# Kernel tuning notes

Hardware: AMD Instinct MI355X
Metric: run time of the kernel (lower is better)

The kernel has to match this reference:

```python
import jax, jax.numpy as jnp
import numpy as np

D_MODEL = 2048
N_HEADS = 32
D_HEAD = 64
CHUNK = 128
SEQ = 2048
BZ = 4
LN_EPS = 1e-5
LAYER_IDX = 12
NUM_LAYERS = 24


def _layernorm(x, scale, bias):
    mu = jnp.mean(x, axis=-1, keepdims=True)
    var = jnp.var(x, axis=-1, keepdims=True)
    return (x - mu) * jax.lax.rsqrt(var + LN_EPS) * scale + bias


def setup_inputs() -> dict:
    key = jax.random.key(0)
    ks = jax.random.split(key, 5)
    a01 = LAYER_IDX / (NUM_LAYERS - 1 + 1e-08)
    a10 = 1.0 - LAYER_IDX / NUM_LAYERS
    decay = -8 + 7 * (np.arange(N_HEADS, dtype=np.float64) / (N_HEADS - 1.0 + 1e-07)) ** (0.7 + 1.3 * a01)
    first = np.full((N_HEADS,), -3.0)
    idx = (np.arange(D_MODEL, dtype=np.float64) / D_MODEL).reshape(1, 1, D_MODEL)
    s = 1.0 / np.sqrt(D_MODEL)
    return {
        'inputs': jax.random.normal(ks[0], (BZ, SEQ, D_MODEL), jnp.float32),
        'time_mix_r': jnp.asarray(idx ** (0.5 * a10), jnp.float32),
        'time_mix_k': jnp.asarray(idx ** a10, jnp.float32),
        'time_mix_v': jnp.asarray(idx ** a10 + 0.3 * a01, jnp.float32),
        'key_weight': jax.random.normal(ks[1], (D_MODEL, D_MODEL), jnp.float32) * s,
        'value_weight': jax.random.normal(ks[2], (D_MODEL, D_MODEL), jnp.float32) * s,
        'receptance_weight': jax.random.normal(ks[3], (D_MODEL, D_MODEL), jnp.float32) * s,
        'output_weight': jax.random.normal(ks[4], (D_MODEL, D_MODEL), jnp.float32) * s,
        'time_decay': jnp.asarray(decay, jnp.float32),
        'time_first': jnp.asarray(first, jnp.float32),
        'ln1_scale': jnp.ones((1, 1, D_MODEL), jnp.float32),
        'ln1_bias': jnp.zeros((1, 1, D_MODEL), jnp.float32),
        'lnx_scale': jnp.ones((N_HEADS, D_HEAD), jnp.float32),
        'lnx_bias': jnp.zeros((N_HEADS, D_HEAD), jnp.float32),
        'chunk_size': CHUNK,
    }


def reference(inputs, time_mix_r, time_mix_k, time_mix_v, key_weight, value_weight,
              receptance_weight, output_weight, time_decay, time_first,
              ln1_scale, ln1_bias, lnx_scale, lnx_bias, chunk_size):
    bz, seq, d = inputs.shape
    H = time_decay.shape[0]
    dh = d // H
    C = chunk_size
    nc = seq // C

    xn = _layernorm(inputs, ln1_scale, ln1_bias)

    # decay machinery (matches the TF w_mask / w_k / w_b construction)
    w = jnp.exp(-jnp.exp(time_decay))                       # (H,)
    rev = jnp.arange(C - 1, -1, -1, dtype=jnp.float32)
    w_pow = w[:, None] ** rev[None, :]                      # (H,C): w^(C-1-j)
    w_k = w_pow[:, None, :]                                 # (H,1,C)
    w_b = w_pow[:, ::-1][:, :, None]                        # (H,C,1): w^i
    w_chunk = (w ** C)[:, None, None]                       # (H,1,1)
    u = jnp.exp(time_first)                                 # (H,)
    ii = jnp.arange(C)
    dmat = ii[:, None] - ii[None, :]                        # i - j
    e = jnp.maximum(dmat - 1, 0)
    w_mask = jnp.where(dmat[None] > 0, w[:, None, None] ** e[None],
                       jnp.where(dmat[None] == 0, u[:, None, None], 0.0))  # (H,C,C)
    w_mask = w_mask[None, None]                             # (1,1,H,C,C)

    # token shift mixing (initial state_x = zeros)
    shift = jnp.concatenate([jnp.zeros((bz, 1, d), xn.dtype), xn[:, :-1]], axis=1)
    rx = xn * time_mix_r + (1.0 - time_mix_r) * shift
    kx = xn * time_mix_k + (1.0 - time_mix_k) * shift
    vx = xn * time_mix_v + (1.0 - time_mix_v) * shift

    r = (rx @ receptance_weight).reshape(bz, nc, C, H, dh).transpose(0, 1, 3, 2, 4)  # (bz,nc,H,C,dh)
    k = (kx @ key_weight).reshape(bz, nc, C, H, dh).transpose(0, 1, 3, 4, 2)         # (bz,nc,H,dh,C)
    v = (vx @ value_weight).reshape(bz, nc, C, H, dh).transpose(0, 1, 3, 2, 4)       # (bz,nc,H,C,dh)

    # intra-chunk attention with decay mask
    rkw = (r @ k) * w_mask                                  # (bz,nc,H,C,C)
    sep = rkw @ v                                           # (bz,nc,H,C,dh)

    # inter-chunk recurrent state via scan
    state0 = jnp.zeros((bz, H, dh, dh), inputs.dtype)

    def step(state, rkv):
        rc, kc, vc = rkv                                    # (bz,H,C,dh),(bz,H,dh,C),(bz,H,C,dh)
        bias = (rc @ state) * w_b                           # (bz,H,C,dh)
        new_state = state * w_chunk + (kc * w_k) @ vc
        return new_state, bias

    r_s = jnp.moveaxis(r, 1, 0)
    k_s = jnp.moveaxis(k, 1, 0)
    v_s = jnp.moveaxis(v, 1, 0)
    state, bias = jax.lax.scan(step, state0, (r_s, k_s, v_s))
    bias = jnp.moveaxis(bias, 0, 1)                         # (bz,nc,H,C,dh)

    att = (sep + bias).transpose(0, 1, 3, 2, 4)             # (bz,nc,C,H,dh)
    att = _layernorm(att, lnx_scale, lnx_bias)              # group norm over dh per head
    out = att.reshape(bz, seq, d) @ output_weight
    return inputs + out, xn[:, -1, :], state
```

## Files before the change

### kernel.cpp

```cpp
#include <hip/hip_runtime.h>

#define D_MODEL 2048
#define N_HEADS 32
#define D_HEAD  64
#define CHUNK   128
#define SEQ     2048
#define BZ      4
#define NC      16
#define NTOK    (BZ*SEQ)
#define LN_EPS  1e-5f

typedef __bf16 bf16_t;
typedef bf16_t bf16x8 __attribute__((ext_vector_type(8)));
typedef float  f32x4  __attribute__((ext_vector_type(4)));

#define GLOBAL_AS __attribute__((address_space(1)))
#define LDS_AS    __attribute__((address_space(3)))

__global__ __launch_bounds__(256) void k_ln_mix(
    const float* __restrict__ x, const float* __restrict__ tmr,
    const float* __restrict__ tmk, const float* __restrict__ tmv,
    const float* __restrict__ g1, const float* __restrict__ b1,
    bf16_t* __restrict__ rxb, bf16_t* __restrict__ kxb, bf16_t* __restrict__ vxb,
    float* __restrict__ xn_last)
{
    __shared__ float sbuf[16];
    const int row = blockIdx.x;
    const int t = row & (SEQ-1);
    const int tid = threadIdx.x;
    const float4* xc4 = (const float4*)(x + (size_t)row*D_MODEL);
    float4 c0 = xc4[tid*2], c1 = xc4[tid*2+1];
    float4 p0 = {0,0,0,0}, p1 = {0,0,0,0};
    const bool hasprev = (t != 0);
    if (hasprev){
        const float4* xp4 = (const float4*)(x + (size_t)(row-1)*D_MODEL);
        p0 = xp4[tid*2]; p1 = xp4[tid*2+1];
    }
    float xc[8] = {c0.x,c0.y,c0.z,c0.w,c1.x,c1.y,c1.z,c1.w};
    float xp[8] = {p0.x,p0.y,p0.z,p0.w,p1.x,p1.y,p1.z,p1.w};
    float sc=0.f, qc=0.f, sp=0.f, qp=0.f;
    for (int q=0;q<8;++q){ sc+=xc[q]; qc+=xc[q]*xc[q]; sp+=xp[q]; qp+=xp[q]*xp[q]; }
    for (int o=1;o<64;o<<=1){
        sc += __shfl_xor(sc,o,64); qc += __shfl_xor(qc,o,64);
        sp += __shfl_xor(sp,o,64); qp += __shfl_xor(qp,o,64);
    }
    const int wave = tid>>6, lane = tid&63;
    if (lane==0){ sbuf[wave*4+0]=sc; sbuf[wave*4+1]=qc; sbuf[wave*4+2]=sp; sbuf[wave*4+3]=qp; }
    __syncthreads();
    sc = sbuf[0]+sbuf[4]+sbuf[8]+sbuf[12];
    qc = sbuf[1]+sbuf[5]+sbuf[9]+sbuf[13];
    sp = sbuf[2]+sbuf[6]+sbuf[10]+sbuf[14];
    qp = sbuf[3]+sbuf[7]+sbuf[11]+sbuf[15];
    const float inv = 1.f/(float)D_MODEL;
    float muc = sc*inv, varc = qc*inv - muc*muc;
    float rc  = rsqrtf(varc + LN_EPS);
    float mup = sp*inv, varp = qp*inv - mup*mup;
    float rp  = rsqrtf(varp + LN_EPS);
    bf16x8 rv, kv, vv;
    const int ci = tid*8;
    float xnl[8];
    for (int q=0;q<8;++q){
        int c = ci+q;
        float gg = g1[c], bb = b1[c];
        float xn = (xc[q]-muc)*rc*gg + bb;
        float sh = hasprev ? ((xp[q]-mup)*rp*gg + bb) : 0.f;
        float mr = tmr[c], mk = tmk[c], mv = tmv[c];
        rv[q] = (bf16_t)(xn*mr + (1.f-mr)*sh);
        kv[q] = (bf16_t)(xn*mk + (1.f-mk)*sh);
        vv[q] = (bf16_t)(xn*mv + (1.f-mv)*sh);
        xnl[q] = xn;
    }
    size_t base = (size_t)row*D_MODEL + ci;
    *(bf16x8*)&rxb[base] = rv;
    *(bf16x8*)&kxb[base] = kv;
    *(bf16x8*)&vxb[base] = vv;
    if (t == SEQ-1){
        int b = row >> 11;
        for (int q=0;q<8;++q) xn_last[(size_t)b*D_MODEL + ci + q] = xnl[q];
    }
}

__global__ __launch_bounds__(256) void k_wt4(
    const float* __restrict__ W0, const float* __restrict__ W1,
    const float* __restrict__ W2, const float* __restrict__ W3,
    bf16_t* __restrict__ WTbase)
{
    __shared__ float tile[64][65];
    const int z = blockIdx.z;
    const float* W = (z==0)?W0:(z==1)?W1:(z==2)?W2:W3;
    bf16_t* WT = WTbase + (size_t)z*D_MODEL*D_MODEL;
    const int n0 = blockIdx.x*64, k0 = blockIdx.y*64;
    const int j = threadIdx.x & 63, i0 = threadIdx.x >> 6;
    for (int it=0; it<16; ++it){
        int i = i0 + it*4;
        tile[j][i] = W[(size_t)(k0+i)*D_MODEL + n0 + j];
    }
    __syncthreads();
    for (int it=0; it<16; ++it){
        int idx = threadIdx.x + it*256;
        int r = idx >> 6, c = idx & 63;
        WT[(size_t)(n0+r)*D_MODEL + k0 + c] = (bf16_t)tile[r][c];
    }
}

__device__ __forceinline__ void xcd_swizzle_8x32(int& bx, int& by)
{
    int id = blockIdx.y*8 + blockIdx.x;
    int p  = id & 7;
    int n  = id >> 3;
    bx = n & 7;
    by = (p<<2) | (n>>3);
}

__device__ __forceinline__ bf16x8 ldfrag(const char* regn, int ks, int row, int quad)
{
    return *(const bf16x8*)(regn + ks*16384 + row*64 + (((quad ^ (row>>1)) & 3) << 4));
}

#define GLD(gp, lp) __builtin_amdgcn_global_load_lds((const GLOBAL_AS void*)(gp), (LDS_AS void*)(lp), 16, 0, 0)
#define STAGE2(gp, lb) do{ GLD((gp), (lb)+tid16); GLD((gp)+rowskip, (lb)+8192+tid16); }while(0)
#define BARX() do{ asm volatile("" ::: "memory"); __builtin_amdgcn_s_barrier(); asm volatile("" ::: "memory"); }while(0)
#define WAITV(n) asm volatile("s_waitcnt vmcnt(" #n ")" ::: "memory")
#define MM(CH) do{ \
    _Pragma("unroll") for (int mf=0;mf<4;++mf){ \
    _Pragma("unroll") for (int nf=0;nf<4;++nf)  \
        acc[mf][(CH)*4+nf] = __builtin_amdgcn_mfma_f32_16x16x32_bf16( \
            a[mf], b[nf], acc[mf][(CH)*4+nf], 0,0,0); } }while(0)

template<int OUT_BF16>
__device__ __forceinline__ void gemm256_core(
    const bf16_t* __restrict__ A, const bf16_t* __restrict__ B,
    void* __restrict__ Cout, const float* __restrict__ resid,
    const int N, const int K, char* smem, int bx, int by)
{
    const int tid = threadIdx.x;
    const int lane = tid&63, quad = lane>>4, l15 = lane&15;
    const int wave = tid>>6;
    const int wm = wave>>1, wn = wave&1;
    const int wrow = wm*64, wcol = wn*128;
    const int arow0 = by*256, bcol0 = bx*256;
    const int NT = K>>6;
    const int K2 = K*2;
    const int tid16 = tid*16;

    const int rr  = tid>>2;
    const int kcb = (((tid&3) ^ ((tid>>3)&3)) << 4);
    const char* Ag = (const char*)A + (size_t)(arow0 + rr)*K2 + kcb;
    const char* Bg = (const char*)B + (size_t)(bcol0 + rr)*K2 + kcb;
    const int rowskip = 128*K2;

    char* A0 = smem;             char* B0 = smem + 32768;
    char* A1 = smem + 65536;     char* B1 = smem + 98304;

    STAGE2(Ag,       A0);
    STAGE2(Bg,       B0);
    STAGE2(Ag + 64,  A0 + 16384);
    STAGE2(Bg + 64,  B0 + 16384);
    STAGE2(Ag + 128, A1);
    WAITV(6);
    BARX();

    f32x4 acc[4][8];
    #pragma unroll
    for (int i=0;i<4;++i)
        #pragma unroll
        for (int j=0;j<8;++j) acc[i][j] = (f32x4){0.f,0.f,0.f,0.f};

    bf16x8 a[4], b[4];

    #pragma unroll 2
    for (int t=0; t<NT; ++t){
        const char* As = (t&1) ? A1 : A0;
        const char* Bs = (t&1) ? B1 : B0;
        char* An = (t&1) ? A0 : A1;
        char* Bn = (t&1) ? B0 : B1;
        char* Ac = (t&1) ? A1 : A0;
        const int tn  = (t+1 < NT) ? t+1 : NT-1;
        const int tn2 = (t+2 < NT) ? t+2 : NT-1;
        const char* gA1 = Ag + tn*128;
        const char* gB1 = Bg + tn*128;
        const char* gA2 = Ag + tn2*128;

        #pragma unroll
        for (int mf=0;mf<4;++mf) a[mf] = ldfrag(As, 0, wrow+mf*16+l15, quad);
        #pragma unroll
        for (int nf=0;nf<4;++nf) b[nf] = ldfrag(Bs, 0, wcol+nf*16+l15, quad);
        STAGE2(gB1, Bn);
        BARX();
        __builtin_amdgcn_s_setprio(1); MM(0); __builtin_amdgcn_s_setprio(0);
        BARX();
        #pragma unroll
        for (int nf=0;nf<4;++nf) b[nf] = ldfrag(Bs, 0, wcol+64+nf*16+l15, quad);
        STAGE2(gA1 + 64, An + 16384);
        WAITV(6);
        BARX();
        __builtin_amdgcn_s_setprio(1); MM(1); __builtin_amdgcn_s_setprio(0);
        BARX();
        #pragma unroll
        for (int mf=0;mf<4;++mf) a[mf] = ldfrag(As, 1, wrow+mf*16+l15, quad);
        #pragma unroll
        for (int nf=0;nf<4;++nf) b[nf] = ldfrag(Bs, 1, wcol+nf*16+l15, quad);
        STAGE2(gB1 + 64, Bn + 16384);
        BARX();
        __builtin_amdgcn_s_setprio(1); MM(0); __builtin_amdgcn_s_setprio(0);
        BARX();
        #pragma unroll
        for (int nf=0;nf<4;++nf) b[nf] = ldfrag(Bs, 1, wcol+64+nf*16+l15, quad);
        STAGE2(gA2, Ac);
        WAITV(6);
        BARX();
        __builtin_amdgcn_s_setprio(1); MM(1); __builtin_amdgcn_s_setprio(0);
        BARX();
    }
    WAITV(0);
    __syncthreads();

    if (OUT_BF16){
        bf16_t* Cb = (bf16_t*)Cout;
        bf16_t* Rp = (bf16_t*)smem;
        #pragma unroll
        for (int jh=0; jh<2; ++jh){
            if (wn == jh){
                #pragma unroll
                for (int mf=0;mf<4;++mf)
                    #pragma unroll
                    for (int nf=0;nf<8;++nf)
                        #pragma unroll
                        for (int e=0;e<4;++e){
                            int rrow = wrow + mf*16 + quad*4 + e;
                            Rp[rrow*136 + nf*16 + l15] = (bf16_t)acc[mf][nf][e];
                        }
            }
            __syncthreads();
            for (int it=0; it<8; ++it){
                int idx = tid + it*512;
                int row = idx >> 4, c8 = (idx & 15)*8;
                *(bf16x8*)&Cb[(size_t)(arow0+row)*N + bcol0 + jh*128 + c8] =
                    *(const bf16x8*)&Rp[row*136 + c8];
            }
            __syncthreads();
        }
    } else {
        float* C = (float*)Cout;
        #pragma unroll
        for (int mf=0;mf<4;++mf)
            #pragma unroll
            for (int nf=0;nf<8;++nf)
                #pragma unroll
                for (int e=0;e<4;++e){
                    size_t r = (size_t)(arow0 + wrow + mf*16 + quad*4 + e);
                    size_t c = (size_t)(bcol0 + wcol + nf*16 + l15);
                    C[r*N + c] = resid[r*N + c] + acc[mf][nf][e];
                }
    }
}

__global__ __launch_bounds__(512, 2) void k_gemm_rkv(
    const bf16_t* __restrict__ Abase, const bf16_t* __restrict__ Bbase,
    bf16_t* __restrict__ Cbase)
{
    __shared__ __align__(16) char smem[131072];
    const int z = blockIdx.z;
    const bf16_t* A = Abase + (size_t)z*NTOK*D_MODEL;
    const bf16_t* B = Bbase + (size_t)z*D_MODEL*D_MODEL;
    bf16_t*       C = Cbase + (size_t)z*NTOK*D_MODEL;
    int bx, by; xcd_swizzle_8x32(bx, by);
    gemm256_core<1>(A, B, (void*)C, nullptr, D_MODEL, D_MODEL, smem, bx, by);
}

__global__ __launch_bounds__(512, 2) void k_gemm_out(
    const bf16_t* __restrict__ A, const bf16_t* __restrict__ B,
    float* __restrict__ C, const float* __restrict__ resid)
{
    __shared__ __align__(16) char smem[131072];
    int bx, by; xcd_swizzle_8x32(bx, by);
    gemm256_core<0>(A, B, (void*)C, resid, D_MODEL, D_MODEL, smem, bx, by);
}

__global__ __launch_bounds__(256) void k_chunk_U(
    const bf16_t* __restrict__ kb, const bf16_t* __restrict__ vb,
    const float* __restrict__ td, float* __restrict__ U)
{
    __shared__ __align__(16) bf16_t kT[64*136];
    __shared__ __align__(16) bf16_t vT[64*136];
    const int bid = blockIdx.x;
    const int h = bid & 31, n = (bid>>5)&15, b = bid>>9;
    const int tid = threadIdx.x;
    const int wave = tid>>6, lane = tid&63, quad = lane>>4, l15 = lane&15;
    const size_t row0 = (size_t)b*SEQ + n*CHUNK;
    const int col0 = h*D_HEAD;
    const float lnw = -__expf(td[h]);
    for (int it=0; it<4; ++it){
        int idx = tid + it*256;
        int row = idx>>3, c8 = (idx&7)*8;
        float wj = __expf(lnw * (float)(CHUNK-1-row));
        bf16x8 kv = *(const bf16x8*)&kb[(row0+row)*D_MODEL + col0 + c8];
        bf16x8 vv = *(const bf16x8*)&vb[(row0+row)*D_MODEL + col0 + c8];
        for (int q=0;q<8;++q){
            kT[(c8+q)*136 + row] = (bf16_t)((float)kv[q] * wj);
            vT[(c8+q)*136 + row] = vv[q];
        }
    }
    __syncthreads();
    f32x4 accU[4];
    for (int j=0;j<4;++j) accU[j] = (f32x4){0.f,0.f,0.f,0.f};
    for (int kk=0; kk<4; ++kk){
        bf16x8 af = *(const bf16x8*)&kT[(wave*16+l15)*136 + kk*32 + quad*8];
        bf16x8 bfr[4];
        for (int j=0;j<4;++j) bfr[j] = *(const bf16x8*)&vT[(j*16+l15)*136 + kk*32 + quad*8];
        for (int j=0;j<4;++j)
            accU[j] = __builtin_amdgcn_mfma_f32_16x16x32_bf16(af, bfr[j], accU[j], 0,0,0);
    }
    float* Ub = U + (size_t)bid*(D_HEAD*D_HEAD);
    for (int j=0;j<4;++j) for (int e=0;e<4;++e){
        int ei = wave*16 + quad*4 + e;
        int d  = j*16 + l15;
        Ub[ei*D_HEAD + d] = accU[j][e];
    }
}

__global__ __launch_bounds__(256) void k_scan(
    const float* __restrict__ U, const float* __restrict__ td,
    bf16_t* __restrict__ stT, float* __restrict__ outState)
{
    const int bh = blockIdx.x;
    const int h = bh & 31, b = bh >> 5;
    const int tid = threadIdx.x;
    const float lnw = -__expf(td[h]);
    const float wC  =  __expf(lnw * (float)CHUNK);
    float st[16];
    for (int q=0;q<16;++q) st[q] = 0.f;
    for (int n=0;n<NC;++n){
        size_t base = ((size_t)((b*NC + n)*N_HEADS + h))*4096;
        for (int q=0;q<16;++q){
            int f = tid + q*256;
            int e = f>>6, d = f&63;
            stT[base + d*64 + e] = (bf16_t)st[q];
            st[q] = st[q]*wC + U[base + f];
        }
    }
    size_t ob = ((size_t)(b*N_HEADS + h))*4096;
    for (int q=0;q<16;++q) outState[ob + tid + q*256] = st[q];
}

__global__ __launch_bounds__(256) void k_att_fused(
    const bf16_t* __restrict__ rb, const bf16_t* __restrict__ kb, const bf16_t* __restrict__ vb,
    const bf16_t* __restrict__ stT, const float* __restrict__ td, const float* __restrict__ tf,
    const float* __restrict__ gx, const float* __restrict__ bx,
    bf16_t* __restrict__ att)
{
    __shared__ __align__(16) char smem[63488];
    bf16_t* rS  = (bf16_t*)smem;
    bf16_t* kS  = (bf16_t*)(smem + 18432);
    bf16_t* vT  = (bf16_t*)(smem + 36864);
    bf16_t* sS  = (bf16_t*)(smem + 54272);
    bf16_t* Sst = kS;
    bf16_t* att_s = kS;
    const int bid = blockIdx.x;
    const int h = bid & 31, n = (bid>>5)&15, b = bid>>9;
    const int tid = threadIdx.x;
    const int wave = tid>>6, lane = tid&63, quad = lane>>4, l15 = lane&15;
    const size_t row0 = (size_t)b*SEQ + n*CHUNK;
    const int col0 = h*D_HEAD;
    const float lnw = -__expf(td[h]);
    const float u   =  __expf(tf[h]);
    for (int it=0; it<4; ++it){
        int idx = tid + it*256;
        int row = idx>>3, c8 = (idx&7)*8;
        *(bf16x8*)&rS[row*72 + c8] = *(const bf16x8*)&rb[(row0+row)*D_MODEL + col0 + c8];
        *(bf16x8*)&kS[row*72 + c8] = *(const bf16x8*)&kb[(row0+row)*D_MODEL + col0 + c8];
        bf16x8 vv = *(const bf16x8*)&vb[(row0+row)*D_MODEL + col0 + c8];
        for (int q=0;q<8;++q) vT[(c8+q)*136 + row] = vv[q];
    }
    const bf16_t* stg = stT + (size_t)bid*4096;
    for (int it=0; it<2; ++it){
        int idx = tid + it*256;
        int row = idx>>3, c8 = (idx&7)*8;
        *(bf16x8*)&sS[row*72 + c8] = *(const bf16x8*)&stg[row*64 + c8];
    }
    __syncthreads();
    f32x4 accS[2][8];
    for (int i=0;i<2;++i) for (int j=0;j<8;++j) accS[i][j] = (f32x4){0.f,0.f,0.f,0.f};
    for (int kk=0; kk<2; ++kk){
        bf16x8 af[2], bfr[8];
        for (int i=0;i<2;++i) af[i] = *(const bf16x8*)&rS[(wave*32+i*16+l15)*72 + kk*32 + quad*8];
        for (int j=0;j<8;++j) bfr[j] = *(const bf16x8*)&kS[(j*16+l15)*72 + kk*32 + quad*8];
        for (int i=0;i<2;++i) for (int j=0;j<8;++j)
            accS[i][j] = __builtin_amdgcn_mfma_f32_16x16x32_bf16(af[i], bfr[j], accS[i][j], 0,0,0);
    }
    __syncthreads();
    f32x4 accP[2][4];
    for (int i=0;i<2;++i) for (int j=0;j<4;++j) accP[i][j] = (f32x4){0.f,0.f,0.f,0.f};
    for (int kk=0; kk<4; ++kk){
        for (int i=0;i<2;++i) for (int jj=0;jj<2;++jj) for (int e=0;e<4;++e){
            int si = wave*32 + i*16 + quad*4 + e;
            int sj = kk*32 + jj*16 + l15;
            float m;
            if (si > sj)       m = __expf(lnw * (float)(si-sj-1));
            else if (si == sj) m = u;
            else               m = 0.f;
            Sst[si*40 + jj*16 + l15] = (bf16_t)(accS[i][kk*2+jj][e] * m);
        }
        __syncthreads();
        bf16x8 af[2], bfr[4];
        for (int i=0;i<2;++i) af[i] = *(const bf16x8*)&Sst[(wave*32+i*16+l15)*40 + quad*8];
        for (int j=0;j<4;++j) bfr[j] = *(const bf16x8*)&vT[(j*16+l15)*136 + kk*32 + quad*8];
        for (int i=0;i<2;++i) for (int j=0;j<4;++j)
            accP[i][j] = __builtin_amdgcn_mfma_f32_16x16x32_bf16(af[i], bfr[j], accP[i][j], 0,0,0);
        __syncthreads();
    }
    f32x4 accB[2][4];
    for (int i=0;i<2;++i) for (int j=0;j<4;++j) accB[i][j] = (f32x4){0.f,0.f,0.f,0.f};
    for (int kk=0; kk<2; ++kk){
        bf16x8 af[2], bfr[4];
        for (int i=0;i<2;++i) af[i] = *(const bf16x8*)&rS[(wave*32+i*16+l15)*72 + kk*32 + quad*8];
        for (int j=0;j<4;++j) bfr[j] = *(const bf16x8*)&sS[(j*16+l15)*72 + kk*32 + quad*8];
        for (int i=0;i<2;++i) for (int j=0;j<4;++j)
            accB[i][j] = __builtin_amdgcn_mfma_f32_16x16x32_bf16(af[i], bfr[j], accB[i][j], 0,0,0);
    }
    float pre[2][4][4];
    float mu_r[2][4], rs_r[2][4];
    for (int i=0;i<2;++i) for (int e=0;e<4;++e){
        int si = wave*32 + i*16 + quad*4 + e;
        float wsi = __expf(lnw * (float)si);
        float s = 0.f, q2 = 0.f;
        for (int j=0;j<4;++j){
            float v = accP[i][j][e] + accB[i][j][e]*wsi;
            pre[i][j][e] = v;
            s += v; q2 += v*v;
        }
        for (int o=1;o<16;o<<=1){ s += __shfl_xor(s,o,64); q2 += __shfl_xor(q2,o,64); }
        float mu = s*(1.f/64.f);
        float var = q2*(1.f/64.f) - mu*mu;
        mu_r[i][e] = mu; rs_r[i][e] = rsqrtf(var + LN_EPS);
    }
    float gxv[4], bxv[4];
    for (int j=0;j<4;++j){ gxv[j] = gx[col0 + j*16 + l15]; bxv[j] = bx[col0 + j*16 + l15]; }
    for (int i=0;i<2;++i) for (int j=0;j<4;++j) for (int e=0;e<4;++e){
        int si = wave*32 + i*16 + quad*4 + e;
        att_s[si*72 + j*16 + l15] = (bf16_t)((pre[i][j][e]-mu_r[i][e])*rs_r[i][e]*gxv[j] + bxv[j]);
    }
    __syncthreads();
    for (int it=0; it<4; ++it){
        int idx = tid + it*256;
        int row = idx>>3, c8 = (idx&7)*8;
        *(bf16x8*)&att[(row0+row)*D_MODEL + col0 + c8] = *(const bf16x8*)&att_s[row*72 + c8];
    }
}

extern "C" void kernel_launch(void* const* d_in, const int* in_sizes, int n_in,
                              void* d_out, int out_size, void* d_ws, size_t ws_size,
                              hipStream_t stream) {
    const float* x   = (const float*)d_in[0];
    const float* tmr = (const float*)d_in[1];
    const float* tmk = (const float*)d_in[2];
    const float* tmv = (const float*)d_in[3];
    const float* Wk  = (const float*)d_in[4];
    const float* Wv  = (const float*)d_in[5];
    const float* Wr  = (const float*)d_in[6];
    const float* Wo  = (const float*)d_in[7];
    const float* td  = (const float*)d_in[8];
    const float* tf  = (const float*)d_in[9];
    const float* g1  = (const float*)d_in[10];
    const float* b1  = (const float*)d_in[11];
    const float* gx  = (const float*)d_in[12];
    const float* bx  = (const float*)d_in[13];

    float* out0 = (float*)d_out;
    float* out1 = out0 + (size_t)NTOK*D_MODEL;
    float* out2 = out1 + (size_t)BZ*D_MODEL;

    const size_t MB = 1ull<<20;
    char* ws = (char*)d_ws;
    bf16_t* rxb = (bf16_t*)(ws);
    bf16_t* kxb = (bf16_t*)(ws + 32*MB);
    bf16_t* vxb = (bf16_t*)(ws + 64*MB);
    bf16_t* WTb = (bf16_t*)(ws + 96*MB);
    bf16_t* WoT = (bf16_t*)(ws + 120*MB);
    bf16_t* rb  = (bf16_t*)(ws + 128*MB);
    float*  U   = (float*)(ws);
    bf16_t* stT = (bf16_t*)(ws + 32*MB);
    bf16_t* att = (bf16_t*)(ws + 64*MB);
    bf16_t* kb  = (bf16_t*)(ws + 160*MB);
    bf16_t* vb  = (bf16_t*)(ws + 192*MB);

    k_ln_mix<<<NTOK, 256, 0, stream>>>(x, tmr, tmk, tmv, g1, b1, rxb, kxb, vxb, out1);

    dim3 gT(32, 32, 4);
    k_wt4<<<gT, 256, 0, stream>>>(Wr, Wk, Wv, Wo, WTb);

    dim3 gG3(D_MODEL/256, NTOK/256, 3);
    k_gemm_rkv<<<gG3, 512, 0, stream>>>(rxb, WTb, rb);

    const int nblk = BZ*NC*N_HEADS;
    k_chunk_U <<<nblk, 256, 0, stream>>>(kb, vb, td, U);
    k_scan    <<<BZ*N_HEADS, 256, 0, stream>>>(U, td, stT, out2);
    k_att_fused<<<nblk, 256, 0, stream>>>(rb, kb, vb, stT, td, tf, gx, bx, att);

    dim3 gG(D_MODEL/256, NTOK/256);
    k_gemm_out<<<gG, 512, 0, stream>>>(att, WoT, out0, x);
}
```

Measured before the change: 602.2 us.

## Double-buffer GEMM register fragments, parallelize scan, precompute decay powers

The GEMM core now double-buffers its A/B fragment registers, loading the next sub-tile's fragments right after each MFMA group so LDS reads overlap matrix math. The state scan is split across twice as many blocks, with vectorized loads and stores, and writes the state untransposed. The attention kernel does that transpose when loading into shared memory instead. It also caches per-head decay powers in a shared-memory table, replacing repeated exp calls. These trade extra register pressure and strided LDS stores for lower latency and better occupancy.

Measured after the change: 554.1 us. 1.09x faster.

```diff
diff --git a/kernel.cpp b/kernel.cpp
--- a/kernel.cpp
+++ b/kernel.cpp
@@ -121,11 +121,17 @@
 #define STAGE2(gp, lb) do{ GLD((gp), (lb)+tid16); GLD((gp)+rowskip, (lb)+8192+tid16); }while(0)
 #define BARX() do{ asm volatile("" ::: "memory"); __builtin_amdgcn_s_barrier(); asm volatile("" ::: "memory"); }while(0)
 #define WAITV(n) asm volatile("s_waitcnt vmcnt(" #n ")" ::: "memory")
-#define MM(CH) do{ \
+#define PFA(dst, buf, ks) do{ _Pragma("unroll") \
+    for (int mf=0;mf<4;++mf) dst[mf] = ldfrag((buf), (ks), wrow+mf*16+l15, quad); }while(0)
+#define PFB(dst, buf, ks, off) do{ _Pragma("unroll") \
+    for (int nf=0;nf<4;++nf) dst[nf] = ldfrag((buf), (ks), wcol+(off)+nf*16+l15, quad); }while(0)
+#define MMX(AV, BV, CH) do{ \
+    __builtin_amdgcn_s_setprio(1); \
     _Pragma("unroll") for (int mf=0;mf<4;++mf){ \
     _Pragma("unroll") for (int nf=0;nf<4;++nf)  \
         acc[mf][(CH)*4+nf] = __builtin_amdgcn_mfma_f32_16x16x32_bf16( \
-            a[mf], b[nf], acc[mf][(CH)*4+nf], 0,0,0); } }while(0)
+            AV[mf], BV[nf], acc[mf][(CH)*4+nf], 0,0,0); } \
+    __builtin_amdgcn_s_setprio(0); }while(0)
 
 template<int OUT_BF16>
 __device__ __forceinline__ void gemm256_core(
@@ -166,7 +172,9 @@
         #pragma unroll
         for (int j=0;j<8;++j) acc[i][j] = (f32x4){0.f,0.f,0.f,0.f};
 
-    bf16x8 a[4], b[4];
+    bf16x8 aP[4], aQ[4], bP[4], bQ[4];
+    PFA(aP, A0, 0);
+    PFB(bP, B0, 0, 0);
 
     #pragma unroll 2
     for (int t=0; t<NT; ++t){
@@ -181,35 +189,29 @@
         const char* gB1 = Bg + tn*128;
         const char* gA2 = Ag + tn2*128;
 
-        #pragma unroll
-        for (int mf=0;mf<4;++mf) a[mf] = ldfrag(As, 0, wrow+mf*16+l15, quad);
-        #pragma unroll
-        for (int nf=0;nf<4;++nf) b[nf] = ldfrag(Bs, 0, wcol+nf*16+l15, quad);
         STAGE2(gB1, Bn);
         BARX();
-        __builtin_amdgcn_s_setprio(1); MM(0); __builtin_amdgcn_s_setprio(0);
-        BARX();
-        #pragma unroll
-        for (int nf=0;nf<4;++nf) b[nf] = ldfrag(Bs, 0, wcol+64+nf*16+l15, quad);
+        MMX(aP, bP, 0);
+        PFB(bQ, Bs, 0, 64);
+        BARX();
         STAGE2(gA1 + 64, An + 16384);
         WAITV(6);
         BARX();
-        __builtin_amdgcn_s_setprio(1); MM(1); __builtin_amdgcn_s_setprio(0);
-        BARX();
-        #pragma unroll
-        for (int mf=0;mf<4;++mf) a[mf] = ldfrag(As, 1, wrow+mf*16+l15, quad);
-        #pragma unroll
-        for (int nf=0;nf<4;++nf) b[nf] = ldfrag(Bs, 1, wcol+nf*16+l15, quad);
+        MMX(aP, bQ, 1);
+        PFA(aQ, As, 1);
+        PFB(bP, Bs, 1, 0);
+        BARX();
         STAGE2(gB1 + 64, Bn + 16384);
         BARX();
-        __builtin_amdgcn_s_setprio(1); MM(0); __builtin_amdgcn_s_setprio(0);
-        BARX();
-        #pragma unroll
-        for (int nf=0;nf<4;++nf) b[nf] = ldfrag(Bs, 1, wcol+64+nf*16+l15, quad);
+        MMX(aQ, bP, 0);
+        PFB(bQ, Bs, 1, 64);
+        BARX();
         STAGE2(gA2, Ac);
         WAITV(6);
         BARX();
-        __builtin_amdgcn_s_setprio(1); MM(1); __builtin_amdgcn_s_setprio(0);
+        MMX(aQ, bQ, 1);
+        PFA(aP, An, 0);
+        PFB(bP, Bn, 0, 0);
         BARX();
     }
     WAITV(0);
@@ -323,24 +325,30 @@
     const float* __restrict__ U, const float* __restrict__ td,
     bf16_t* __restrict__ stT, float* __restrict__ outState)
 {
-    const int bh = blockIdx.x;
+    const int blk = blockIdx.x;
+    const int bh = blk >> 1, sl = blk & 1;
     const int h = bh & 31, b = bh >> 5;
-    const int tid = threadIdx.x;
+    const int f8 = (sl*256 + threadIdx.x)*8;
     const float lnw = -__expf(td[h]);
     const float wC  =  __expf(lnw * (float)CHUNK);
-    float st[16];
-    for (int q=0;q<16;++q) st[q] = 0.f;
+    float st[8];
+    #pragma unroll
+    for (int q=0;q<8;++q) st[q] = 0.f;
     for (int n=0;n<NC;++n){
         size_t base = ((size_t)((b*NC + n)*N_HEADS + h))*4096;
-        for (int q=0;q<16;++q){
-            int f = tid + q*256;
-            int e = f>>6, d = f&63;
-            stT[base + d*64 + e] = (bf16_t)st[q];
-            st[q] = st[q]*wC + U[base + f];
-        }
-    }
-    size_t ob = ((size_t)(b*N_HEADS + h))*4096;
-    for (int q=0;q<16;++q) outState[ob + tid + q*256] = st[q];
+        bf16x8 s8;
+        #pragma unroll
+        for (int q=0;q<8;++q) s8[q] = (bf16_t)st[q];
+        *(bf16x8*)&stT[base + f8] = s8;
+        float4 u0 = *(const float4*)&U[base + f8];
+        float4 u1 = *(const float4*)&U[base + f8 + 4];
+        float uu[8] = {u0.x,u0.y,u0.z,u0.w,u1.x,u1.y,u1.z,u1.w};
+        #pragma unroll
+        for (int q=0;q<8;++q) st[q] = st[q]*wC + uu[q];
+    }
+    size_t ob = ((size_t)(b*N_HEADS + h))*4096 + f8;
+    #pragma unroll
+    for (int q=0;q<8;++q) outState[ob + q] = st[q];
 }
 
 __global__ __launch_bounds__(256) void k_att_fused(
@@ -349,11 +357,12 @@
     const float* __restrict__ gx, const float* __restrict__ bx,
     bf16_t* __restrict__ att)
 {
-    __shared__ __align__(16) char smem[63488];
+    __shared__ __align__(16) char smem[64000];
     bf16_t* rS  = (bf16_t*)smem;
     bf16_t* kS  = (bf16_t*)(smem + 18432);
     bf16_t* vT  = (bf16_t*)(smem + 36864);
     bf16_t* sS  = (bf16_t*)(smem + 54272);
+    float*  wpS = (float*)(smem + 63488);
     bf16_t* Sst = kS;
     bf16_t* att_s = kS;
     const int bid = blockIdx.x;
@@ -364,6 +373,7 @@
     const int col0 = h*D_HEAD;
     const float lnw = -__expf(td[h]);
     const float u   =  __expf(tf[h]);
+    if (tid < 128) wpS[tid] = __expf(lnw * (float)tid);
     for (int it=0; it<4; ++it){
         int idx = tid + it*256;
         int row = idx>>3, c8 = (idx&7)*8;
@@ -376,7 +386,8 @@
     for (int it=0; it<2; ++it){
         int idx = tid + it*256;
         int row = idx>>3, c8 = (idx&7)*8;
-        *(bf16x8*)&sS[row*72 + c8] = *(const bf16x8*)&stg[row*64 + c8];
+        bf16x8 sv = *(const bf16x8*)&stg[row*64 + c8];
+        for (int q=0;q<8;++q) sS[(c8+q)*72 + row] = sv[q];
     }
     __syncthreads();
     f32x4 accS[2][8];
@@ -396,7 +407,7 @@
             int si = wave*32 + i*16 + quad*4 + e;
             int sj = kk*32 + jj*16 + l15;
             float m;
-            if (si > sj)       m = __expf(lnw * (float)(si-sj-1));
+            if (si > sj)       m = wpS[si-sj-1];
             else if (si == sj) m = u;
             else               m = 0.f;
             Sst[si*40 + jj*16 + l15] = (bf16_t)(accS[i][kk*2+jj][e] * m);
@@ -422,7 +433,7 @@
     float mu_r[2][4], rs_r[2][4];
     for (int i=0;i<2;++i) for (int e=0;e<4;++e){
         int si = wave*32 + i*16 + quad*4 + e;
-        float wsi = __expf(lnw * (float)si);
+        float wsi = wpS[si];
         float s = 0.f, q2 = 0.f;
         for (int j=0;j<4;++j){
             float v = accP[i][j][e] + accB[i][j][e]*wsi;
@@ -494,7 +505,7 @@
 
     const int nblk = BZ*NC*N_HEADS;
     k_chunk_U <<<nblk, 256, 0, stream>>>(kb, vb, td, U);
-    k_scan    <<<BZ*N_HEADS, 256, 0, stream>>>(U, td, stT, out2);
+    k_scan    <<<256, 256, 0, stream>>>(U, td, stT, out2);
     k_att_fused<<<nblk, 256, 0, stream>>>(rb, kb, vb, stT, td, tf, gx, bx, att);
 
     dim3 gG(D_MODEL/256, NTOK/256);
```
